# Performance work log

Hardware: AMD Instinct MI355X
Metric: run time of the kernel (lower is better)

## Reference

```python
import jax, jax.numpy as jnp
import numpy as np

SLOT_SIZE = 64
START_IDX = 0  # slot2idx['<start>']
STOP_IDX = 1   # slot2idx['<stop>']
NEG_INF = -10000.0


def setup_inputs() -> dict:
    key = jax.random.key(0)
    k1, k2 = jax.random.split(key)
    B, T, S = 512, 512, SLOT_SIZE
    logits = jax.random.normal(k1, (B, T, S), dtype=jnp.float32)
    masks = jnp.ones((B, T), dtype=jnp.float32)
    # nn.Parameter(torch.randn(S, S)) with START/STOP constraints from __init__
    transitions = jax.random.normal(k2, (S, S), dtype=jnp.float32)
    transitions = transitions.at[START_IDX, :].set(NEG_INF)
    transitions = transitions.at[:, STOP_IDX].set(NEG_INF)
    return {"logits": logits, "masks": masks, "transitions": transitions}


def reference(logits, masks, transitions):
    """Faithful CRF.forward == _viterbi_decode(logits, masks).

    Replicates the original quirks:
      - masks multiply only the emission feat (transitions are NOT masked
        inside the Viterbi recursion);
      - path_score is taken from the LAST next_tag's (next_tag = S-1)
        score vector at the final timestep, and the backtrace is seeded
        from that same column's argmax;
      - the backtrace re-applies the last backpointer table once before
        walking backwards (exactly as the torch loop does), and the
        popped start tag is dropped, giving a (B, T-1) path.
    """
    B, T, S = logits.shape
    init = jnp.full((B, S), NEG_INF, dtype=logits.dtype).at[:, START_IDX].set(0.0)

    # masked emissions for timesteps 1..T-1, time-major for scan: (T-1, B, S)
    feats = jnp.swapaxes(logits[:, 1:, :] * masks[:, 1:, None], 0, 1)

    def step(fv, feat_t):
        # scores[b, next, prev] = fv[b, prev] + transitions[next, prev]
        scores = fv[:, None, :] + transitions[None, :, :]  # (B, S, S)
        bptr = jnp.argmax(scores, axis=2).astype(jnp.int32)  # (B, S)
        vmax = jnp.max(scores, axis=2)                       # (B, S)
        return vmax + feat_t, (bptr, vmax)

    _, (bptrs, vmaxs) = jax.lax.scan(step, init, feats)  # (T-1, B, S) each

    # torch quirk: next_tag_var / best_tag_id left over from next_tag = S-1
    path_score = vmaxs[-1][:, S - 1]          # (B,)
    t0 = bptrs[-1][:, S - 1]                  # (B,) seed for backtrace

    def back(tag, bp):
        new_tag = jnp.take_along_axis(bp, tag[:, None], axis=1)[:, 0]
        return new_tag, tag  # emit the tag BEFORE following the pointer

    # reverse scan walks bptrs from last to first; emitted ys land at their
    # original time index, so ys == reversed best_path (start tag dropped
    # because the final carry -- the start tag -- is never emitted).
    _, ys = jax.lax.scan(back, t0, bptrs, reverse=True)  # (T-1, B)
    best_seq = jnp.swapaxes(ys, 0, 1)  # (B, T-1)
    return path_score, best_seq
```

## Files before the change

### kernel.cpp

```cpp
#include <hip/hip_runtime.h>


constexpr int Bz = 512;
constexpr int Tz = 512;
constexpr int Sz = 64;
constexpr float NEGINF = -10000.0f;

__device__ __forceinline__ float rlf(float x, int lane) {
    return __int_as_float(__builtin_amdgcn_readlane(__float_as_int(x), lane));
}

__device__ __forceinline__ void lds_barrier() {
    asm volatile("s_waitcnt lgkmcnt(0)\n\ts_barrier" ::: "memory");
}

__global__ __launch_bounds__(256)
void crf_viterbi_kernel(const float* __restrict__ logits,
                        const float* __restrict__ masks,
                        const float* __restrict__ trans,
                        float* __restrict__ out)
{
    const int n  = threadIdx.x & 63;
    const int w  = __builtin_amdgcn_readfirstlane(threadIdx.x >> 6);
    const int b  = blockIdx.x;
    const int pb = 16 * w;
    const int tg = n ^ pb;

    __shared__ unsigned bp[128 * 64];
    __shared__ float pval[2][4][64];
    __shared__ int   pidx[2][4][64];
    __shared__ float ys[Tz - 1];

    float tr[16];
    {
        const float4* tr4 = reinterpret_cast<const float4*>(trans + tg * 64 + pb);
        #pragma unroll
        for (int k = 0; k < 4; ++k) {
            float4 t = tr4[k];
            tr[4 * k + 0] = t.x; tr[4 * k + 1] = t.y;
            tr[4 * k + 2] = t.z; tr[4 * k + 3] = t.w;
        }
    }

    float fv = (tg == 0) ? 0.0f : NEGINF;

    const float* lgbase = logits + (size_t)b * Tz * Sz;
    const float* mkbase = masks + (size_t)b * Tz;

    float lgc[4], lgn[4], mkc[4], mkn[4];
    #pragma unroll
    for (int k = 0; k < 4; ++k) {
        lgc[k] = lgbase[(1 + k) * Sz + tg];
        mkc[k] = mkbase[1 + k];
        lgn[k] = lgbase[(5 + k) * Sz + tg];
        mkn[k] = mkbase[5 + k];
    }

    unsigned pk = 0;
    float psc = 0.0f;

    auto step = [&](int k, float lg, float mk) {
        const int buf = k & 1;
        float v[16];
        #pragma unroll
        for (int j = 0; j < 16; ++j)
            v[j] = rlf(fv, j) + tr[j];

        float mv[8]; int mi[8];
        #pragma unroll
        for (int c = 0; c < 8; ++c) {
            bool g = v[2 * c + 1] > v[2 * c];
            mv[c] = g ? v[2 * c + 1] : v[2 * c];
            mi[c] = g ? (2 * c + 1) : (2 * c);
        }
        #pragma unroll
        for (int st = 1; st < 8; st <<= 1) {
            #pragma unroll
            for (int c = 0; c < 8; c += 2 * st) {
                bool g = mv[c + st] > mv[c];
                mv[c] = g ? mv[c + st] : mv[c];
                mi[c] = g ? mi[c + st] : mi[c];
            }
        }
        pval[buf][w][tg] = mv[0];
        pidx[buf][w][tg] = pb + mi[0];

        lds_barrier();

        float c0 = pval[buf][0][tg], c1 = pval[buf][1][tg];
        float c2 = pval[buf][2][tg], c3 = pval[buf][3][tg];
        int   j0 = pidx[buf][0][tg], j1 = pidx[buf][1][tg];
        int   j2 = pidx[buf][2][tg], j3 = pidx[buf][3][tg];
        bool g1 = c1 > c0;  float m01 = g1 ? c1 : c0;  int k01 = g1 ? j1 : j0;
        bool g3 = c3 > c2;  float m23 = g3 ? c3 : c2;  int k23 = g3 ? j3 : j2;
        bool gm = m23 > m01;
        float m  = gm ? m23 : m01;
        int   gi = gm ? k23 : k01;

        pk |= ((unsigned)gi) << (8 * k);
        fv = m + lg * mk;
        return m;
    };

    for (int g = 0; g < 127; ++g) {
        step(0, lgc[0], mkc[0]);
        step(1, lgc[1], mkc[1]);
        step(2, lgc[2], mkc[2]);
        step(3, lgc[3], mkc[3]);

        if (w == 0) bp[g * 64 + n] = pk;
        pk = 0;

        #pragma unroll
        for (int k = 0; k < 4; ++k) { lgc[k] = lgn[k]; mkc[k] = mkn[k]; }
        #pragma unroll
        for (int k = 0; k < 4; ++k) {
            int t = 4 * g + 9 + k;
            t = (t < Tz) ? t : (Tz - 1);
            lgn[k] = lgbase[t * Sz + tg];
            mkn[k] = mkbase[t];
        }
    }

    step(0, lgc[0], mkc[0]);
    step(1, lgc[1], mkc[1]);
    float mlast = step(2, lgc[2], mkc[2]);
    psc = mlast;

    if (w == 0) {
        bp[127 * 64 + n] = pk;
        if (n == 63) out[b] = psc;
    }
    __syncthreads();

    if (w == 0) {
        unsigned wcur = bp[127 * 64 + n];
        int w127_63 = __builtin_amdgcn_readlane((int)wcur, 63);
        int tag = (w127_63 >> 16) & 255;

        for (int g = 127; g >= 0; --g) {
            unsigned wnext = (g > 0) ? bp[(g - 1) * 64 + n] : 0u;
            int smax = (g == 127) ? 2 : 3;
            for (int s = smax; s >= 0; --s) {
                int idx = 4 * g + s;
                if (n == 0) ys[idx] = (float)tag;
                int wd = __builtin_amdgcn_readlane((int)wcur, tag);
                tag = (wd >> (8 * s)) & 255;
            }
            wcur = wnext;
        }
    }
    __syncthreads();

    float* outseq = out + Bz + (size_t)b * (Tz - 1);
    for (int k = threadIdx.x; k < Tz - 1; k += 256) outseq[k] = ys[k];
}

extern "C" void kernel_launch(void* const* d_in, const int* in_sizes, int n_in,
                              void* d_out, int out_size, void* d_ws, size_t ws_size,
                              hipStream_t stream) {
    const float* logits = (const float*)d_in[0];
    const float* masks  = (const float*)d_in[1];
    const float* trans  = (const float*)d_in[2];
    float* out = (float*)d_out;
    (void)in_sizes; (void)n_in; (void)out_size; (void)d_ws; (void)ws_size;

    crf_viterbi_kernel<<<dim3(Bz), dim3(256), 0, stream>>>(logits, masks, trans, out);
}
```

Measured before the change: 343.2 us.

## Use one wavefront per batch row, removing cross-wave LDS reduction and barriers

Each batch row now runs on a single 64-lane wavefront, where every lane holds a full row of 64 transition values and does the max/argmax over all 64 previous tags alone. Before, four waves each reduced 16 tags and merged the results through LDS with a barrier at every timestep. Dropping that removes the per-step barrier and LDS round-trip from the serial recursion. In exchange each step does four times as many readlane and compare operations per wave, and the per-lane register count goes up.

```diff
diff --git a/kernel.cpp b/kernel.cpp
--- a/kernel.cpp
+++ b/kernel.cpp
@@ -10,39 +10,30 @@
     return __int_as_float(__builtin_amdgcn_readlane(__float_as_int(x), lane));
 }
 
-__device__ __forceinline__ void lds_barrier() {
-    asm volatile("s_waitcnt lgkmcnt(0)\n\ts_barrier" ::: "memory");
-}
-
-__global__ __launch_bounds__(256)
+__global__ __launch_bounds__(64)
 void crf_viterbi_kernel(const float* __restrict__ logits,
                         const float* __restrict__ masks,
                         const float* __restrict__ trans,
                         float* __restrict__ out)
 {
-    const int n  = threadIdx.x & 63;
-    const int w  = __builtin_amdgcn_readfirstlane(threadIdx.x >> 6);
-    const int b  = blockIdx.x;
-    const int pb = 16 * w;
-    const int tg = n ^ pb;
+    const int n = threadIdx.x;
+    const int b = blockIdx.x;
 
     __shared__ unsigned bp[128 * 64];
-    __shared__ float pval[2][4][64];
-    __shared__ int   pidx[2][4][64];
     __shared__ float ys[Tz - 1];
 
-    float tr[16];
+    float tr[64];
     {
-        const float4* tr4 = reinterpret_cast<const float4*>(trans + tg * 64 + pb);
+        const float4* tr4 = reinterpret_cast<const float4*>(trans + (size_t)n * Sz);
         #pragma unroll
-        for (int k = 0; k < 4; ++k) {
+        for (int k = 0; k < 16; ++k) {
             float4 t = tr4[k];
             tr[4 * k + 0] = t.x; tr[4 * k + 1] = t.y;
             tr[4 * k + 2] = t.z; tr[4 * k + 3] = t.w;
         }
     }
 
-    float fv = (tg == 0) ? 0.0f : NEGINF;
+    float fv = (n == 0) ? 0.0f : NEGINF;
 
     const float* lgbase = logits + (size_t)b * Tz * Sz;
     const float* mkbase = masks + (size_t)b * Tz;
@@ -50,56 +41,42 @@
     float lgc[4], lgn[4], mkc[4], mkn[4];
     #pragma unroll
     for (int k = 0; k < 4; ++k) {
-        lgc[k] = lgbase[(1 + k) * Sz + tg];
+        lgc[k] = lgbase[(1 + k) * Sz + n];
         mkc[k] = mkbase[1 + k];
-        lgn[k] = lgbase[(5 + k) * Sz + tg];
+        lgn[k] = lgbase[(5 + k) * Sz + n];
         mkn[k] = mkbase[5 + k];
     }
 
     unsigned pk = 0;
-    float psc = 0.0f;
 
-    auto step = [&](int k, float lg, float mk) {
-        const int buf = k & 1;
-        float v[16];
-        #pragma unroll
-        for (int j = 0; j < 16; ++j)
-            v[j] = rlf(fv, j) + tr[j];
-
-        float mv[8]; int mi[8];
+    auto step = [&](int k, float lg, float mk) -> float {
+        float m[8]; int id[8];
         #pragma unroll
         for (int c = 0; c < 8; ++c) {
-            bool g = v[2 * c + 1] > v[2 * c];
-            mv[c] = g ? v[2 * c + 1] : v[2 * c];
-            mi[c] = g ? (2 * c + 1) : (2 * c);
+            m[c]  = rlf(fv, 8 * c) + tr[8 * c];
+            id[c] = 8 * c;
+            #pragma unroll
+            for (int j = 1; j < 8; ++j) {
+                const int p = 8 * c + j;
+                float cand = rlf(fv, p) + tr[p];
+                bool g = cand > m[c];
+                id[c] = g ? p : id[c];
+                m[c]  = fmaxf(m[c], cand);
+            }
         }
         #pragma unroll
         for (int st = 1; st < 8; st <<= 1) {
             #pragma unroll
             for (int c = 0; c < 8; c += 2 * st) {
-                bool g = mv[c + st] > mv[c];
-                mv[c] = g ? mv[c + st] : mv[c];
-                mi[c] = g ? mi[c + st] : mi[c];
+                bool g = m[c + st] > m[c];
+                id[c] = g ? id[c + st] : id[c];
+                m[c]  = fmaxf(m[c], m[c + st]);
             }
         }
-        pval[buf][w][tg] = mv[0];
-        pidx[buf][w][tg] = pb + mi[0];
-
-        lds_barrier();
-
-        float c0 = pval[buf][0][tg], c1 = pval[buf][1][tg];
-        float c2 = pval[buf][2][tg], c3 = pval[buf][3][tg];
-        int   j0 = pidx[buf][0][tg], j1 = pidx[buf][1][tg];
-        int   j2 = pidx[buf][2][tg], j3 = pidx[buf][3][tg];
-        bool g1 = c1 > c0;  float m01 = g1 ? c1 : c0;  int k01 = g1 ? j1 : j0;
-        bool g3 = c3 > c2;  float m23 = g3 ? c3 : c2;  int k23 = g3 ? j3 : j2;
-        bool gm = m23 > m01;
-        float m  = gm ? m23 : m01;
-        int   gi = gm ? k23 : k01;
-
-        pk |= ((unsigned)gi) << (8 * k);
-        fv = m + lg * mk;
-        return m;
+        pk |= ((unsigned)id[0]) << (8 * k);
+        float mm = m[0];
+        fv = mm + lg * mk;
+        return mm;
     };
 
     for (int g = 0; g < 127; ++g) {
@@ -108,7 +85,7 @@
         step(2, lgc[2], mkc[2]);
         step(3, lgc[3], mkc[3]);
 
-        if (w == 0) bp[g * 64 + n] = pk;
+        bp[g * 64 + n] = pk;
         pk = 0;
 
         #pragma unroll
@@ -117,43 +94,36 @@
         for (int k = 0; k < 4; ++k) {
             int t = 4 * g + 9 + k;
             t = (t < Tz) ? t : (Tz - 1);
-            lgn[k] = lgbase[t * Sz + tg];
+            lgn[k] = lgbase[t * Sz + n];
             mkn[k] = mkbase[t];
         }
     }
 
     step(0, lgc[0], mkc[0]);
     step(1, lgc[1], mkc[1]);
-    float mlast = step(2, lgc[2], mkc[2]);
-    psc = mlast;
+    float psc = step(2, lgc[2], mkc[2]);
+    bp[127 * 64 + n] = pk;
+    if (n == 63) out[b] = psc;
 
-    if (w == 0) {
-        bp[127 * 64 + n] = pk;
-        if (n == 63) out[b] = psc;
+    unsigned wcur = bp[127 * 64 + n];
+    int w127_63 = __builtin_amdgcn_readlane((int)wcur, 63);
+    int tag = (w127_63 >> 16) & 255;
+
+    for (int g = 127; g >= 0; --g) {
+        unsigned wnext = (g > 0) ? bp[(g - 1) * 64 + n] : 0u;
+        const int smax = (g == 127) ? 2 : 3;
+        for (int s = smax; s >= 0; --s) {
+            int idx = 4 * g + s;
+            if (n == 0) ys[idx] = (float)tag;
+            int wd = __builtin_amdgcn_readlane((int)wcur, tag);
+            tag = (wd >> (8 * s)) & 255;
+        }
+        wcur = wnext;
     }
+
     __syncthreads();
-
-    if (w == 0) {
-        unsigned wcur = bp[127 * 64 + n];
-        int w127_63 = __builtin_amdgcn_readlane((int)wcur, 63);
-        int tag = (w127_63 >> 16) & 255;
-
-        for (int g = 127; g >= 0; --g) {
-            unsigned wnext = (g > 0) ? bp[(g - 1) * 64 + n] : 0u;
-            int smax = (g == 127) ? 2 : 3;
-            for (int s = smax; s >= 0; --s) {
-                int idx = 4 * g + s;
-                if (n == 0) ys[idx] = (float)tag;
-                int wd = __builtin_amdgcn_readlane((int)wcur, tag);
-                tag = (wd >> (8 * s)) & 255;
-            }
-            wcur = wnext;
-        }
-    }
-    __syncthreads();
-
     float* outseq = out + Bz + (size_t)b * (Tz - 1);
-    for (int k = threadIdx.x; k < Tz - 1; k += 256) outseq[k] = ys[k];
+    for (int k = n; k < Tz - 1; k += 64) outseq[k] = ys[k];
 }
 
 extern "C" void kernel_launch(void* const* d_in, const int* in_sizes, int n_in,
@@ -165,5 +135,5 @@
     float* out = (float*)d_out;
     (void)in_sizes; (void)n_in; (void)out_size; (void)d_ws; (void)ws_size;
 
-    crf_viterbi_kernel<<<dim3(Bz), dim3(256), 0, stream>>>(logits, masks, trans, out);
+    crf_viterbi_kernel<<<dim3(Bz), dim3(64), 0, stream>>>(logits, masks, trans, out);
 }
```

New measurement: 425.8 us. 24.0% more time.

## Process two batch rows per block to interleave independent Viterbi chains

Applied to the files above, without the earlier changes.

Each block now runs two independent batch rows, interleaving their per-step readlane/max phases so that a single LDS barrier per timestep serves both chains and one chain's work hides the other's latency. The grid halves to 256 blocks, and waves_per_eu(1,1) lets the compiler use more registers. The backtrace for the second row runs on wave 1, in parallel with wave 0. This trades fewer blocks and a doubled LDS footprint for instruction-level parallelism inside the serial recurrence.

```diff
diff --git a/kernel.cpp b/kernel.cpp
--- a/kernel.cpp
+++ b/kernel.cpp
@@ -4,6 +4,7 @@
 constexpr int Bz = 512;
 constexpr int Tz = 512;
 constexpr int Sz = 64;
+constexpr int GRID = Bz / 2;
 constexpr float NEGINF = -10000.0f;
 
 __device__ __forceinline__ float rlf(float x, int lane) {
@@ -15,6 +16,7 @@
 }
 
 __global__ __launch_bounds__(256)
+__attribute__((amdgpu_waves_per_eu(1, 1)))
 void crf_viterbi_kernel(const float* __restrict__ logits,
                         const float* __restrict__ masks,
                         const float* __restrict__ trans,
@@ -22,14 +24,17 @@
 {
     const int n  = threadIdx.x & 63;
     const int w  = __builtin_amdgcn_readfirstlane(threadIdx.x >> 6);
-    const int b  = blockIdx.x;
     const int pb = 16 * w;
     const int tg = n ^ pb;
-
-    __shared__ unsigned bp[128 * 64];
-    __shared__ float pval[2][4][64];
-    __shared__ int   pidx[2][4][64];
-    __shared__ float ys[Tz - 1];
+    const int bA = blockIdx.x;
+    const int bB = blockIdx.x + GRID;
+
+    __shared__ unsigned bpA[128 * 64];
+    __shared__ unsigned bpB[128 * 64];
+    __shared__ float pvalA[2][4][64];  __shared__ int pidxA[2][4][64];
+    __shared__ float pvalB[2][4][64];  __shared__ int pidxB[2][4][64];
+    __shared__ float ysA[Tz - 1];
+    __shared__ float ysB[Tz - 1];
 
     float tr[16];
     {
@@ -42,29 +47,35 @@
         }
     }
 
-    float fv = (tg == 0) ? 0.0f : NEGINF;
-
-    const float* lgbase = logits + (size_t)b * Tz * Sz;
-    const float* mkbase = masks + (size_t)b * Tz;
-
-    float lgc[4], lgn[4], mkc[4], mkn[4];
+    float fvA = (tg == 0) ? 0.0f : NEGINF;
+    float fvB = (tg == 0) ? 0.0f : NEGINF;
+
+    const float* lgbA = logits + (size_t)bA * Tz * Sz;
+    const float* lgbB = logits + (size_t)bB * Tz * Sz;
+    const float* mkbA = masks + (size_t)bA * Tz;
+    const float* mkbB = masks + (size_t)bB * Tz;
+
+    float lgcA[4], lgnA[4], mkcA[4], mknA[4];
+    float lgcB[4], lgnB[4], mkcB[4], mknB[4];
     #pragma unroll
     for (int k = 0; k < 4; ++k) {
-        lgc[k] = lgbase[(1 + k) * Sz + tg];
-        mkc[k] = mkbase[1 + k];
-        lgn[k] = lgbase[(5 + k) * Sz + tg];
-        mkn[k] = mkbase[5 + k];
-    }
-
-    unsigned pk = 0;
-    float psc = 0.0f;
-
-    auto step = [&](int k, float lg, float mk) {
+        lgcA[k] = lgbA[(1 + k) * Sz + tg];  mkcA[k] = mkbA[1 + k];
+        lgnA[k] = lgbA[(5 + k) * Sz + tg];  mknA[k] = mkbA[5 + k];
+        lgcB[k] = lgbB[(1 + k) * Sz + tg];  mkcB[k] = mkbB[1 + k];
+        lgnB[k] = lgbB[(5 + k) * Sz + tg];  mknB[k] = mkbB[5 + k];
+    }
+
+    unsigned pkA = 0, pkB = 0;
+
+    auto phase1 = [&](int k, float fv, float (&pval)[2][4][64], int (&pidx)[2][4][64]) {
         const int buf = k & 1;
+        float s[16];
+        #pragma unroll
+        for (int j = 0; j < 16; ++j) s[j] = rlf(fv, j);
+        __builtin_amdgcn_sched_barrier(0);
         float v[16];
         #pragma unroll
-        for (int j = 0; j < 16; ++j)
-            v[j] = rlf(fv, j) + tr[j];
+        for (int j = 0; j < 16; ++j) v[j] = s[j] + tr[j];
 
         float mv[8]; int mi[8];
         #pragma unroll
@@ -84,9 +95,11 @@
         }
         pval[buf][w][tg] = mv[0];
         pidx[buf][w][tg] = pb + mi[0];
-
-        lds_barrier();
-
+    };
+
+    auto phase2 = [&](int k, float (&pval)[2][4][64], int (&pidx)[2][4][64],
+                      float lg, float mk, float& fv, unsigned& pk) -> float {
+        const int buf = k & 1;
         float c0 = pval[buf][0][tg], c1 = pval[buf][1][tg];
         float c2 = pval[buf][2][tg], c3 = pval[buf][3][tg];
         int   j0 = pidx[buf][0][tg], j1 = pidx[buf][1][tg];
@@ -96,64 +109,96 @@
         bool gm = m23 > m01;
         float m  = gm ? m23 : m01;
         int   gi = gm ? k23 : k01;
-
         pk |= ((unsigned)gi) << (8 * k);
         fv = m + lg * mk;
         return m;
     };
 
+    auto steppair = [&](int k) {
+        phase1(k, fvA, pvalA, pidxA);
+        phase1(k, fvB, pvalB, pidxB);
+        lds_barrier();
+        phase2(k, pvalA, pidxA, lgcA[k], mkcA[k], fvA, pkA);
+        phase2(k, pvalB, pidxB, lgcB[k], mkcB[k], fvB, pkB);
+    };
+
     for (int g = 0; g < 127; ++g) {
-        step(0, lgc[0], mkc[0]);
-        step(1, lgc[1], mkc[1]);
-        step(2, lgc[2], mkc[2]);
-        step(3, lgc[3], mkc[3]);
-
-        if (w == 0) bp[g * 64 + n] = pk;
-        pk = 0;
-
-        #pragma unroll
-        for (int k = 0; k < 4; ++k) { lgc[k] = lgn[k]; mkc[k] = mkn[k]; }
+        steppair(0); steppair(1); steppair(2); steppair(3);
+
+        if (w == 0) {
+            bpA[g * 64 + n] = pkA;
+            bpB[g * 64 + n] = pkB;
+        }
+        pkA = 0; pkB = 0;
+
+        #pragma unroll
+        for (int k = 0; k < 4; ++k) {
+            lgcA[k] = lgnA[k]; mkcA[k] = mknA[k];
+            lgcB[k] = lgnB[k]; mkcB[k] = mknB[k];
+        }
         #pragma unroll
         for (int k = 0; k < 4; ++k) {
             int t = 4 * g + 9 + k;
             t = (t < Tz) ? t : (Tz - 1);
-            lgn[k] = lgbase[t * Sz + tg];
-            mkn[k] = mkbase[t];
-        }
-    }
-
-    step(0, lgc[0], mkc[0]);
-    step(1, lgc[1], mkc[1]);
-    float mlast = step(2, lgc[2], mkc[2]);
-    psc = mlast;
+            lgnA[k] = lgbA[t * Sz + tg];  mknA[k] = mkbA[t];
+            lgnB[k] = lgbB[t * Sz + tg];  mknB[k] = mkbB[t];
+        }
+    }
+
+    steppair(0); steppair(1);
+    phase1(2, fvA, pvalA, pidxA);
+    phase1(2, fvB, pvalB, pidxB);
+    lds_barrier();
+    float pscA = phase2(2, pvalA, pidxA, lgcA[2], mkcA[2], fvA, pkA);
+    float pscB = phase2(2, pvalB, pidxB, lgcB[2], mkcB[2], fvB, pkB);
 
     if (w == 0) {
-        bp[127 * 64 + n] = pk;
-        if (n == 63) out[b] = psc;
+        bpA[127 * 64 + n] = pkA;
+        bpB[127 * 64 + n] = pkB;
+        if (n == 63) {
+            out[bA] = pscA;
+            out[bB] = pscB;
+        }
     }
     __syncthreads();
 
     if (w == 0) {
-        unsigned wcur = bp[127 * 64 + n];
-        int w127_63 = __builtin_amdgcn_readlane((int)wcur, 63);
-        int tag = (w127_63 >> 16) & 255;
-
+        unsigned wcur = bpA[127 * 64 + n];
+        int tag = (__builtin_amdgcn_readlane((int)wcur, 63) >> 16) & 255;
         for (int g = 127; g >= 0; --g) {
-            unsigned wnext = (g > 0) ? bp[(g - 1) * 64 + n] : 0u;
-            int smax = (g == 127) ? 2 : 3;
+            unsigned wnext = (g > 0) ? bpA[(g - 1) * 64 + n] : 0u;
+            const int smax = (g == 127) ? 2 : 3;
             for (int s = smax; s >= 0; --s) {
                 int idx = 4 * g + s;
-                if (n == 0) ys[idx] = (float)tag;
+                if (n == 0) ysA[idx] = (float)tag;
                 int wd = __builtin_amdgcn_readlane((int)wcur, tag);
                 tag = (wd >> (8 * s)) & 255;
             }
             wcur = wnext;
         }
+    } else if (w == 1) {
+        unsigned wcur = bpB[127 * 64 + n];
+        int tag = (__builtin_amdgcn_readlane((int)wcur, 63) >> 16) & 255;
+        for (int g = 127; g >= 0; --g) {
+            unsigned wnext = (g > 0) ? bpB[(g - 1) * 64 + n] : 0u;
+            const int smax = (g == 127) ? 2 : 3;
+            for (int s = smax; s >= 0; --s) {
+                int idx = 4 * g + s;
+                if (n == 0) ysB[idx] = (float)tag;
+                int wd = __builtin_amdgcn_readlane((int)wcur, tag);
+                tag = (wd >> (8 * s)) & 255;
+            }
+            wcur = wnext;
+        }
     }
     __syncthreads();
 
-    float* outseq = out + Bz + (size_t)b * (Tz - 1);
-    for (int k = threadIdx.x; k < Tz - 1; k += 256) outseq[k] = ys[k];
+    float* oA = out + Bz + (size_t)bA * (Tz - 1);
+    float* oB = out + Bz + (size_t)bB * (Tz - 1);
+    for (int k = threadIdx.x; k < Tz - 1; k += 256) {
+        oA[k] = ysA[k];
+        oB[k] = ysB[k];
+    }
 }
 
 extern "C" void kernel_launch(void* const* d_in, const int* in_sizes, int n_in,
@@ -165,5 +210,5 @@
     float* out = (float*)d_out;
     (void)in_sizes; (void)n_in; (void)out_size; (void)d_ws; (void)ws_size;
 
-    crf_viterbi_kernel<<<dim3(Bz), dim3(256), 0, stream>>>(logits, masks, trans, out);
-}
+    crf_viterbi_kernel<<<dim3(GRID), dim3(256), 0, stream>>>(logits, masks, trans, out);
+}
```

Measured after the change: 416.6 us. +21.4%, slower.
